# Kernel tuning notes

Measured on AMD Instinct MI355X. Metric: run time of the kernel, lower is better.

Reference implementation:

```python
import jax, jax.numpy as jnp
import numpy as np

N, D, H = 8192, 256, 128
KEEP_RATIO = 0.5
TEMP = 1.0
COS_EPS = 1e-4  # torch CosineSimilarity eps
NEG = -9e15


def setup_inputs() -> dict:
    key = jax.random.key(0)
    k1, k2, k3, k4 = jax.random.split(key, 4)
    features = jax.random.normal(k1, (N, D), dtype=jnp.float32)
    adj = jax.random.randint(k2, (N, N), 0, 2, dtype=jnp.int32)
    # module init: Linear weights ~ N(0, 0.001)
    Wq = jax.random.normal(k3, (H, D), dtype=jnp.float32) * 0.001
    Wk = jax.random.normal(k4, (H, D), dtype=jnp.float32) * 0.001
    return {"features": features, "adj": adj, "Wq": Wq, "Wk": Wk}


def _cos_normalize(x):
    # torch cosine: x / max(||x||, eps)
    n = jnp.linalg.norm(x, axis=-1, keepdims=True)
    return x / jnp.maximum(n, COS_EPS)


def reference(features, adj, Wq, Wk):
    # projections [N, H]
    Qn = _cos_normalize(features @ Wq.T)
    Kn = _cos_normalize(features @ Wk.T)
    # raw_att[i, j] = cos(Wq f_j, Wk f_i)  -> [N, N]
    raw_att = Kn @ Qn.T
    att = jnp.where(adj > 0, raw_att, NEG) * TEMP
    att = jax.nn.softmax(att, axis=1)
    prop_fea = att @ features  # [N, D]
    # nodes with no neighbors keep their own features
    adj_mask = (jnp.sum(adj, axis=1) > 0).astype(features.dtype)[:, None]
    prop_fea = adj_mask * prop_fea + (1.0 - adj_mask) * features
    # gate=None branch: fixed keep_ratio mixing
    return (1.0 - KEEP_RATIO) * prop_fea + KEEP_RATIO * features
```

## Files before the change

kernel.cpp:

```cpp
#include <hip/hip_runtime.h>
#include <stdint.h>
#include <stddef.h>

#define NN 8192
#define DD 256
#define HH 128

typedef short bf16x8 __attribute__((ext_vector_type(8)));
typedef float f32x4  __attribute__((ext_vector_type(4)));
typedef int   i32x4  __attribute__((ext_vector_type(4)));

static __device__ __forceinline__ short f2bf(float x){
  unsigned u = __float_as_uint(x);
  u = (u + 0x7FFFu + ((u >> 16) & 1u)) >> 16;
  return (short)(unsigned short)u;
}

static __device__ __forceinline__ bf16x8 cvt8(const float* p){
  f32x4 a = *(const f32x4*)p;
  f32x4 b = *(const f32x4*)(p + 4);
  bf16x8 o;
  o[0]=f2bf(a[0]); o[1]=f2bf(a[1]); o[2]=f2bf(a[2]); o[3]=f2bf(a[3]);
  o[4]=f2bf(b[0]); o[5]=f2bf(b[1]); o[6]=f2bf(b[2]); o[7]=f2bf(b[3]);
  return o;
}

static __device__ __forceinline__ bf16x8 ld16(const void* p){
  i32x4 v = *(const i32x4*)p;
  return __builtin_bit_cast(bf16x8, v);
}

__global__ __launch_bounds__(256) void k_transpose(const float* __restrict__ f,
                                                   unsigned short* __restrict__ ft){
  __shared__ unsigned short tile[64][65];
  int t  = threadIdx.x;
  int i0 = blockIdx.x * 64, d0 = blockIdx.y * 64;
  int r0 = t >> 6, c = t & 63;
  for (int it = 0; it < 16; ++it){
    int r = r0 + it * 4;
    tile[c][r] = (unsigned short)f2bf(f[(size_t)(i0 + r) * DD + d0 + c]);
  }
  __syncthreads();
  for (int it = 0; it < 16; ++it){
    int rr = r0 + it * 4;
    ft[(size_t)(d0 + rr) * NN + i0 + c] = tile[rr][c];
  }
}

__global__ __launch_bounds__(256) void k_proj(const float* __restrict__ f,
                                              const float* __restrict__ Wq,
                                              const float* __restrict__ Wk,
                                              unsigned short* __restrict__ Qn,
                                              unsigned short* __restrict__ Kn){
  int t = threadIdx.x, wave = t >> 6, l = t & 63;
  int i0 = blockIdx.x * 64 + wave * 16;
  int lr = l & 15, lk = l >> 4;
  bf16x8 ka[8];
  for (int ks = 0; ks < 8; ++ks)
    ka[ks] = cvt8(f + (size_t)(i0 + lr) * DD + ks * 32 + lk * 8);
  for (int pj = 0; pj < 2; ++pj){
    const float* W = pj ? Wk : Wq;
    unsigned short* out = pj ? Kn : Qn;
    f32x4 acc[8];
    for (int n = 0; n < 8; ++n) acc[n] = (f32x4){0.f,0.f,0.f,0.f};
    for (int ks = 0; ks < 8; ++ks)
      for (int n = 0; n < 8; ++n){
        bf16x8 bb = cvt8(W + (size_t)(n * 16 + lr) * DD + ks * 32 + lk * 8);
        acc[n] = __builtin_amdgcn_mfma_f32_16x16x32_bf16(ka[ks], bb, acc[n], 0, 0, 0);
      }
    for (int r = 0; r < 4; ++r){
      float n2 = 0.f;
      for (int n = 0; n < 8; ++n){ float v = acc[n][r]; n2 += v * v; }
      n2 += __shfl_xor(n2, 1); n2 += __shfl_xor(n2, 2);
      n2 += __shfl_xor(n2, 4); n2 += __shfl_xor(n2, 8);
      float s = 1.f / fmaxf(sqrtf(n2), 1e-4f);
      int row = i0 + lk * 4 + r;
      for (int n = 0; n < 8; ++n)
        out[(size_t)row * HH + n * 16 + lr] = (unsigned short)f2bf(acc[n][r] * s);
    }
  }
}

__global__ __launch_bounds__(256, 2) void k_attn(const int* __restrict__ adj,
      const unsigned short* __restrict__ Qn, const unsigned short* __restrict__ Kn,
      const unsigned short* __restrict__ ft,
      float* __restrict__ num_p, float* __restrict__ den_p){
  __shared__ __align__(16) char smem[57344];
  char* qn_s = smem;
  char* ft_s = smem + 16384;
  char* w_s  = smem + 49152;
  int t = threadIdx.x, wave = t >> 6, l = t & 63;
  int ib = blockIdx.x >> 2, js = blockIdx.x & 3;
  int i0 = ib * 64;
  int jbase = js * 2048;
  int lr = l & 15, lk = l >> 4;
  int swz = (l & 7) << 4;
  bf16x8 ka[4];
  {
    const unsigned short* kp = Kn + (size_t)(i0 + wave * 16 + lr) * HH;
    for (int ks = 0; ks < 4; ++ks) ka[ks] = ld16(kp + ks * 32 + lk * 8);
  }
  f32x4 pv[2][8];
  for (int a = 0; a < 2; ++a) for (int b = 0; b < 8; ++b) pv[a][b] = (f32x4){0.f,0.f,0.f,0.f};
  float dacc[4] = {0.f, 0.f, 0.f, 0.f};
  int rgp = wave & 1, dh = wave >> 1;
  int qrow = t >> 4, qc = t & 15;
  int frow = t >> 3, fc = t & 7;

  for (int step = 0; step < 32; ++step){
    int j0 = jbase + step * 64;
    __syncthreads();
    for (int it = 0; it < 4; ++it){
      int r = qrow + it * 16;
      i32x4 v = *(const i32x4*)(Qn + (size_t)(j0 + r) * HH + qc * 8);
      *(i32x4*)(qn_s + r * 256 + ((qc * 16) ^ ((r & 7) << 4))) = v;
    }
    for (int it = 0; it < 8; ++it){
      int d2 = frow + it * 32;
      i32x4 v = *(const i32x4*)(ft + (size_t)d2 * NN + j0 + fc * 8);
      *(i32x4*)(ft_s + d2 * 128 + ((fc * 16) ^ ((d2 & 7) << 4))) = v;
    }
    int adjv[4][4];
    for (int r = 0; r < 4; ++r){
      const int* ap = adj + (size_t)(i0 + wave * 16 + lk * 4 + r) * NN + j0 + lr;
      for (int cg = 0; cg < 4; ++cg)
        adjv[cg][r] = __builtin_nontemporal_load(ap + cg * 16);
    }
    __syncthreads();
    f32x4 sa[4];
    for (int cg = 0; cg < 4; ++cg) sa[cg] = (f32x4){0.f,0.f,0.f,0.f};
    for (int ks = 0; ks < 4; ++ks){
      int kb = (ks * 64 + lk * 16) ^ swz;
      for (int cg = 0; cg < 4; ++cg){
        bf16x8 bq = ld16(qn_s + (cg * 16 + lr) * 256 + kb);
        sa[cg] = __builtin_amdgcn_mfma_f32_16x16x32_bf16(ka[ks], bq, sa[cg], 0, 0, 0);
      }
    }
    for (int cg = 0; cg < 4; ++cg)
      for (int r = 0; r < 4; ++r){
        float w = adjv[cg][r] > 0 ? __expf(sa[cg][r]) : 0.f;
        dacc[r] += w;
        int row = wave * 16 + lk * 4 + r;
        *(unsigned short*)(w_s + row * 128 + ((cg * 32 + lr * 2) ^ ((row & 7) << 4)))
            = (unsigned short)f2bf(w);
      }
    __syncthreads();
    for (int ks = 0; ks < 2; ++ks){
      int kb = (ks * 64 + lk * 16) ^ swz;
      bf16x8 a0 = ld16(w_s + (rgp * 32 + lr) * 128 + kb);
      bf16x8 a1 = ld16(w_s + (rgp * 32 + 16 + lr) * 128 + kb);
      for (int dn = 0; dn < 8; ++dn){
        int dl = dh * 128 + dn * 16 + lr;
        bf16x8 bv = ld16(ft_s + dl * 128 + kb);
        pv[0][dn] = __builtin_amdgcn_mfma_f32_16x16x32_bf16(a0, bv, pv[0][dn], 0, 0, 0);
        pv[1][dn] = __builtin_amdgcn_mfma_f32_16x16x32_bf16(a1, bv, pv[1][dn], 0, 0, 0);
      }
    }
  }
  for (int r = 0; r < 4; ++r){
    float v = dacc[r];
    v += __shfl_xor(v, 1); v += __shfl_xor(v, 2);
    v += __shfl_xor(v, 4); v += __shfl_xor(v, 8);
    if (lr == 0) den_p[(size_t)js * NN + i0 + wave * 16 + lk * 4 + r] = v;
  }
  float* np = num_p + (size_t)js * NN * DD;
  for (int rgi = 0; rgi < 2; ++rgi)
    for (int dn = 0; dn < 8; ++dn)
      for (int r = 0; r < 4; ++r){
        int row = i0 + rgp * 32 + rgi * 16 + lk * 4 + r;
        int col = dh * 128 + dn * 16 + lr;
        np[(size_t)row * DD + col] = pv[rgi][dn][r];
      }
}

__global__ __launch_bounds__(256) void k_final(const float* __restrict__ num_p,
                                               const float* __restrict__ den_p,
                                               const float* __restrict__ f,
                                               float* __restrict__ out){
  int gid = blockIdx.x * 256 + threadIdx.x;
  int i = gid >> 6;
  f32x4 nv = (f32x4){0.f,0.f,0.f,0.f};
  float dv = 0.f;
  for (int s = 0; s < 4; ++s){
    nv += *(const f32x4*)(num_p + (size_t)s * NN * DD + (size_t)gid * 4);
    dv += den_p[(size_t)s * NN + i];
  }
  f32x4 fv = *(const f32x4*)(f + (size_t)gid * 4);
  f32x4 o;
  if (dv > 0.f){
    float inv = 0.5f / dv;
    o = nv * inv + fv * 0.5f;
  } else {
    o = fv;
  }
  *(f32x4*)(out + (size_t)gid * 4) = o;
}

extern "C" void kernel_launch(void* const* d_in, const int* in_sizes, int n_in,
                              void* d_out, int out_size, void* d_ws, size_t ws_size,
                              hipStream_t stream){
  (void)in_sizes; (void)n_in; (void)out_size;
  const float* feat = (const float*)d_in[0];
  const int*   adj  = (const int*)d_in[1];
  const float* Wq   = (const float*)d_in[2];
  const float* Wk   = (const float*)d_in[3];
  float* out = (float*)d_out;
  char* ws = (char*)d_ws;
  unsigned short* Qn = (unsigned short*)(ws);
  unsigned short* Kn = (unsigned short*)(ws + (2u << 20));
  unsigned short* ft = (unsigned short*)(ws + (4u << 20));
  float* num_p = (float*)(ws + (8u << 20));
  float* den_p = (float*)(ws + (40u << 20));
  if (ws_size < (40u << 20) + (4u * NN * 4u)) return;

  k_transpose<<<dim3(128, 4), 256, 0, stream>>>(feat, ft);
  k_proj<<<128, 256, 0, stream>>>(feat, Wq, Wk, Qn, Kn);
  k_attn<<<512, 256, 0, stream>>>(adj, Qn, Kn, ft, num_p, den_p);
  k_final<<<2048, 256, 0, stream>>>(num_p, den_p, feat, out);
}
```

Baseline: 233.0 us.

## Pre-fragment Q and features for direct MFMA loads and double-buffer adj

Qn and the transposed features are written in MFMA-fragment order so the attention kernel loads its operands straight from global memory into registers, dropping the per-step LDS staging of Q and features. The kernel switches to 32x32x16 MFMA tiles, keeps only the probability tile in shared memory, and prefetches the next step's adj values into a second register buffer. The denominator partials are split per j-group, so eight slices are written instead of four. The aim is to cut LDS traffic and barrier stalls and to hide adj load latency, at the cost of more registers and uncoalesced reads from global memory or L2.

```diff
diff --git a/kernel.cpp b/kernel.cpp
--- a/kernel.cpp
+++ b/kernel.cpp
@@ -6,16 +6,16 @@
 #define DD 256
 #define HH 128
 
-typedef short bf16x8 __attribute__((ext_vector_type(8)));
-typedef float f32x4  __attribute__((ext_vector_type(4)));
-typedef int   i32x4  __attribute__((ext_vector_type(4)));
+typedef short bf16x8  __attribute__((ext_vector_type(8)));
+typedef float f32x4   __attribute__((ext_vector_type(4)));
+typedef float f32x16  __attribute__((ext_vector_type(16)));
+typedef int   i32x4   __attribute__((ext_vector_type(4)));
 
 static __device__ __forceinline__ short f2bf(float x){
   unsigned u = __float_as_uint(x);
   u = (u + 0x7FFFu + ((u >> 16) & 1u)) >> 16;
   return (short)(unsigned short)u;
 }
-
 static __device__ __forceinline__ bf16x8 cvt8(const float* p){
   f32x4 a = *(const f32x4*)p;
   f32x4 b = *(const f32x4*)(p + 4);
@@ -24,153 +24,169 @@
   o[4]=f2bf(b[0]); o[5]=f2bf(b[1]); o[6]=f2bf(b[2]); o[7]=f2bf(b[3]);
   return o;
 }
-
 static __device__ __forceinline__ bf16x8 ld16(const void* p){
   i32x4 v = *(const i32x4*)p;
   return __builtin_bit_cast(bf16x8, v);
 }
 
-__global__ __launch_bounds__(256) void k_transpose(const float* __restrict__ f,
-                                                   unsigned short* __restrict__ ft){
-  __shared__ unsigned short tile[64][65];
-  int t  = threadIdx.x;
-  int i0 = blockIdx.x * 64, d0 = blockIdx.y * 64;
-  int r0 = t >> 6, c = t & 63;
-  for (int it = 0; it < 16; ++it){
-    int r = r0 + it * 4;
-    tile[c][r] = (unsigned short)f2bf(f[(size_t)(i0 + r) * DD + d0 + c]);
-  }
-  __syncthreads();
-  for (int it = 0; it < 16; ++it){
-    int rr = r0 + it * 4;
-    ft[(size_t)(d0 + rr) * NN + i0 + c] = tile[rr][c];
-  }
+__global__ __launch_bounds__(256) void k_ftfrag(const float* __restrict__ f,
+                                                unsigned short* __restrict__ ftf){
+  int t = threadIdx.x;
+  int fr = blockIdx.x * 4 + (t >> 6);
+  int l  = t & 63;
+  int jt = fr >> 3, dt = fr & 7;
+  int j = jt * 16 + (l >> 5) * 8, d = dt * 32 + (l & 31);
+  bf16x8 o;
+  #pragma unroll
+  for (int e = 0; e < 8; ++e) o[e] = f2bf(f[(size_t)(j + e) * DD + d]);
+  *(bf16x8*)(ftf + (size_t)fr * 512 + l * 8) = o;
 }
 
 __global__ __launch_bounds__(256) void k_proj(const float* __restrict__ f,
                                               const float* __restrict__ Wq,
                                               const float* __restrict__ Wk,
-                                              unsigned short* __restrict__ Qn,
+                                              unsigned short* __restrict__ Qnf,
                                               unsigned short* __restrict__ Kn){
   int t = threadIdx.x, wave = t >> 6, l = t & 63;
   int i0 = blockIdx.x * 64 + wave * 16;
   int lr = l & 15, lk = l >> 4;
   bf16x8 ka[8];
+  #pragma unroll
   for (int ks = 0; ks < 8; ++ks)
     ka[ks] = cvt8(f + (size_t)(i0 + lr) * DD + ks * 32 + lk * 8);
   for (int pj = 0; pj < 2; ++pj){
     const float* W = pj ? Wk : Wq;
-    unsigned short* out = pj ? Kn : Qn;
     f32x4 acc[8];
+    #pragma unroll
     for (int n = 0; n < 8; ++n) acc[n] = (f32x4){0.f,0.f,0.f,0.f};
     for (int ks = 0; ks < 8; ++ks)
+      #pragma unroll
       for (int n = 0; n < 8; ++n){
         bf16x8 bb = cvt8(W + (size_t)(n * 16 + lr) * DD + ks * 32 + lk * 8);
         acc[n] = __builtin_amdgcn_mfma_f32_16x16x32_bf16(ka[ks], bb, acc[n], 0, 0, 0);
       }
+    #pragma unroll
     for (int r = 0; r < 4; ++r){
       float n2 = 0.f;
+      #pragma unroll
       for (int n = 0; n < 8; ++n){ float v = acc[n][r]; n2 += v * v; }
       n2 += __shfl_xor(n2, 1); n2 += __shfl_xor(n2, 2);
       n2 += __shfl_xor(n2, 4); n2 += __shfl_xor(n2, 8);
       float s = 1.f / fmaxf(sqrtf(n2), 1e-4f);
       int row = i0 + lk * 4 + r;
-      for (int n = 0; n < 8; ++n)
-        out[(size_t)row * HH + n * 16 + lr] = (unsigned short)f2bf(acc[n][r] * s);
+      #pragma unroll
+      for (int n = 0; n < 8; ++n){
+        short v = f2bf(acc[n][r] * s);
+        if (pj){
+          Kn[(size_t)row * HH + n * 16 + lr] = (unsigned short)v;
+        } else {
+          size_t off = ((size_t)(row >> 5) * 8 + n) * 512
+                     + ((row & 31) + 32 * (lr >> 3)) * 8 + (lr & 7);
+          Qnf[off] = (unsigned short)v;
+        }
+      }
     }
   }
 }
 
-__global__ __launch_bounds__(256, 2) void k_attn(const int* __restrict__ adj,
-      const unsigned short* __restrict__ Qn, const unsigned short* __restrict__ Kn,
-      const unsigned short* __restrict__ ft,
+#define STEP(CUR, NXT, SS) {                                                      \
+  const int j0 = jbase + (SS) * 64;                                               \
+  const int jn = ((SS) < 31) ? j0 + 64 : j0;                                      \
+  _Pragma("unroll")                                                               \
+  for (int r = 0; r < 16; ++r)                                                    \
+    NXT[r] = __builtin_nontemporal_load(                                          \
+        adj + (size_t)(iA + (r & 3) + 8 * (r >> 2)) * NN + jn + jg * 32 + lc);    \
+  f32x16 st;                                                                      \
+  _Pragma("unroll") for (int e = 0; e < 16; ++e) st[e] = 0.f;                     \
+  { const unsigned short* qb = Qnf + ((size_t)((j0 + jg * 32) >> 5) * 8) * 512 + (size_t)l * 8; \
+    _Pragma("unroll")                                                             \
+    for (int hs = 0; hs < 8; ++hs)                                                \
+      st = __builtin_amdgcn_mfma_f32_32x32x16_bf16(kb[hs], ld16(qb + hs * 512), st, 0, 0, 0); } \
+  bf16x8 bv[8];                                                                   \
+  { const unsigned short* fb = ftf + ((size_t)(j0 >> 4) * 8 + wq * 2) * 512 + (size_t)l * 8; \
+    _Pragma("unroll")                                                             \
+    for (int ks = 0; ks < 4; ++ks){                                               \
+      bv[ks * 2]     = ld16(fb + ks * 4096);                                      \
+      bv[ks * 2 + 1] = ld16(fb + ks * 4096 + 512); } }                            \
+  _Pragma("unroll")                                                               \
+  for (int r = 0; r < 16; ++r){                                                   \
+    float wv = (CUR[r] > 0) ? __expf(st[r]) : 0.f;          \
+    dacc[r] += wv;                                                                \
+    int row = ig * 32 + (r & 3) + 8 * (r >> 2) + 4 * h;                           \
+    int byo = row * 128 + (((jg * 32 + lc) * 2) ^ ((row & 7) << 4));              \
+    *(unsigned short*)(p_lds + byo) = (unsigned short)f2bf(wv);                   \
+  }                                                                               \
+  __syncthreads();                                                                \
+  _Pragma("unroll")                                                               \
+  for (int ks = 0; ks < 4; ++ks){                                                 \
+    int ko = (ks * 32 + h * 16) ^ ((lc & 7) << 4);                                \
+    bf16x8 pa0 = ld16(p_lds + lc * 128 + ko);                                     \
+    bf16x8 pa1 = ld16(p_lds + (32 + lc) * 128 + ko);                              \
+    pv00 = __builtin_amdgcn_mfma_f32_32x32x16_bf16(pa0, bv[ks*2],   pv00, 0,0,0); \
+    pv01 = __builtin_amdgcn_mfma_f32_32x32x16_bf16(pa0, bv[ks*2+1], pv01, 0,0,0); \
+    pv10 = __builtin_amdgcn_mfma_f32_32x32x16_bf16(pa1, bv[ks*2],   pv10, 0,0,0); \
+    pv11 = __builtin_amdgcn_mfma_f32_32x32x16_bf16(pa1, bv[ks*2+1], pv11, 0,0,0); \
+  }                                                                               \
+  __syncthreads();                                                                \
+}
+
+__global__ __launch_bounds__(256, 2) void k_attn(
+      const int* __restrict__ adj,
+      const unsigned short* __restrict__ Qnf, const unsigned short* __restrict__ Kn,
+      const unsigned short* __restrict__ ftf,
       float* __restrict__ num_p, float* __restrict__ den_p){
-  __shared__ __align__(16) char smem[57344];
-  char* qn_s = smem;
-  char* ft_s = smem + 16384;
-  char* w_s  = smem + 49152;
+  __shared__ __attribute__((aligned(16))) char p_lds[8192];
   int t = threadIdx.x, wave = t >> 6, l = t & 63;
+  int lc = l & 31, h = l >> 5;
+  int ig = wave >> 1, jg = wave & 1, wq = wave;
   int ib = blockIdx.x >> 2, js = blockIdx.x & 3;
   int i0 = ib * 64;
   int jbase = js * 2048;
-  int lr = l & 15, lk = l >> 4;
-  int swz = (l & 7) << 4;
-  bf16x8 ka[4];
-  {
-    const unsigned short* kp = Kn + (size_t)(i0 + wave * 16 + lr) * HH;
-    for (int ks = 0; ks < 4; ++ks) ka[ks] = ld16(kp + ks * 32 + lk * 8);
-  }
-  f32x4 pv[2][8];
-  for (int a = 0; a < 2; ++a) for (int b = 0; b < 8; ++b) pv[a][b] = (f32x4){0.f,0.f,0.f,0.f};
-  float dacc[4] = {0.f, 0.f, 0.f, 0.f};
-  int rgp = wave & 1, dh = wave >> 1;
-  int qrow = t >> 4, qc = t & 15;
-  int frow = t >> 3, fc = t & 7;
-
-  for (int step = 0; step < 32; ++step){
-    int j0 = jbase + step * 64;
-    __syncthreads();
-    for (int it = 0; it < 4; ++it){
-      int r = qrow + it * 16;
-      i32x4 v = *(const i32x4*)(Qn + (size_t)(j0 + r) * HH + qc * 8);
-      *(i32x4*)(qn_s + r * 256 + ((qc * 16) ^ ((r & 7) << 4))) = v;
+  int iA = i0 + ig * 32 + 4 * h;
+
+  bf16x8 kb[8];
+  { const unsigned short* kp = Kn + (size_t)(i0 + ig * 32 + lc) * HH + h * 8;
+    #pragma unroll
+    for (int hs = 0; hs < 8; ++hs) kb[hs] = ld16(kp + hs * 16); }
+
+  f32x16 pv00, pv01, pv10, pv11;
+  #pragma unroll
+  for (int e = 0; e < 16; ++e){ pv00[e]=0.f; pv01[e]=0.f; pv10[e]=0.f; pv11[e]=0.f; }
+  float dacc[16];
+  #pragma unroll
+  for (int r = 0; r < 16; ++r) dacc[r] = 0.f;
+
+  int adjA[16], adjB[16];
+  #pragma unroll
+  for (int r = 0; r < 16; ++r)
+    adjA[r] = __builtin_nontemporal_load(
+        adj + (size_t)(iA + (r & 3) + 8 * (r >> 2)) * NN + jbase + jg * 32 + lc);
+
+  for (int sp = 0; sp < 16; ++sp){
+    STEP(adjA, adjB, 2 * sp)
+    STEP(adjB, adjA, 2 * sp + 1)
+  }
+
+  #pragma unroll
+  for (int r = 0; r < 16; ++r){
+    float v = dacc[r];
+    v += __shfl_xor(v, 1); v += __shfl_xor(v, 2); v += __shfl_xor(v, 4);
+    v += __shfl_xor(v, 8); v += __shfl_xor(v, 16);
+    if (lc == 0){
+      int i = i0 + ig * 32 + (r & 3) + 8 * (r >> 2) + 4 * h;
+      den_p[(size_t)(js * 2 + jg) * NN + i] = v;
     }
-    for (int it = 0; it < 8; ++it){
-      int d2 = frow + it * 32;
-      i32x4 v = *(const i32x4*)(ft + (size_t)d2 * NN + j0 + fc * 8);
-      *(i32x4*)(ft_s + d2 * 128 + ((fc * 16) ^ ((d2 & 7) << 4))) = v;
-    }
-    int adjv[4][4];
-    for (int r = 0; r < 4; ++r){
-      const int* ap = adj + (size_t)(i0 + wave * 16 + lk * 4 + r) * NN + j0 + lr;
-      for (int cg = 0; cg < 4; ++cg)
-        adjv[cg][r] = __builtin_nontemporal_load(ap + cg * 16);
-    }
-    __syncthreads();
-    f32x4 sa[4];
-    for (int cg = 0; cg < 4; ++cg) sa[cg] = (f32x4){0.f,0.f,0.f,0.f};
-    for (int ks = 0; ks < 4; ++ks){
-      int kb = (ks * 64 + lk * 16) ^ swz;
-      for (int cg = 0; cg < 4; ++cg){
-        bf16x8 bq = ld16(qn_s + (cg * 16 + lr) * 256 + kb);
-        sa[cg] = __builtin_amdgcn_mfma_f32_16x16x32_bf16(ka[ks], bq, sa[cg], 0, 0, 0);
-      }
-    }
-    for (int cg = 0; cg < 4; ++cg)
-      for (int r = 0; r < 4; ++r){
-        float w = adjv[cg][r] > 0 ? __expf(sa[cg][r]) : 0.f;
-        dacc[r] += w;
-        int row = wave * 16 + lk * 4 + r;
-        *(unsigned short*)(w_s + row * 128 + ((cg * 32 + lr * 2) ^ ((row & 7) << 4)))
-            = (unsigned short)f2bf(w);
-      }
-    __syncthreads();
-    for (int ks = 0; ks < 2; ++ks){
-      int kb = (ks * 64 + lk * 16) ^ swz;
-      bf16x8 a0 = ld16(w_s + (rgp * 32 + lr) * 128 + kb);
-      bf16x8 a1 = ld16(w_s + (rgp * 32 + 16 + lr) * 128 + kb);
-      for (int dn = 0; dn < 8; ++dn){
-        int dl = dh * 128 + dn * 16 + lr;
-        bf16x8 bv = ld16(ft_s + dl * 128 + kb);
-        pv[0][dn] = __builtin_amdgcn_mfma_f32_16x16x32_bf16(a0, bv, pv[0][dn], 0, 0, 0);
-        pv[1][dn] = __builtin_amdgcn_mfma_f32_16x16x32_bf16(a1, bv, pv[1][dn], 0, 0, 0);
-      }
-    }
-  }
-  for (int r = 0; r < 4; ++r){
-    float v = dacc[r];
-    v += __shfl_xor(v, 1); v += __shfl_xor(v, 2);
-    v += __shfl_xor(v, 4); v += __shfl_xor(v, 8);
-    if (lr == 0) den_p[(size_t)js * NN + i0 + wave * 16 + lk * 4 + r] = v;
   }
   float* np = num_p + (size_t)js * NN * DD;
-  for (int rgi = 0; rgi < 2; ++rgi)
-    for (int dn = 0; dn < 8; ++dn)
-      for (int r = 0; r < 4; ++r){
-        int row = i0 + rgp * 32 + rgi * 16 + lk * 4 + r;
-        int col = dh * 128 + dn * 16 + lr;
-        np[(size_t)row * DD + col] = pv[rgi][dn][r];
-      }
+  #pragma unroll
+  for (int r = 0; r < 16; ++r){
+    int i = i0 + (r & 3) + 8 * (r >> 2) + 4 * h;
+    int d = wq * 64 + lc;
+    np[(size_t)i * DD + d]             = pv00[r];
+    np[(size_t)i * DD + d + 32]        = pv01[r];
+    np[(size_t)(i + 32) * DD + d]      = pv10[r];
+    np[(size_t)(i + 32) * DD + d + 32] = pv11[r];
+  }
 }
 
 __global__ __launch_bounds__(256) void k_final(const float* __restrict__ num_p,
@@ -181,10 +197,12 @@
   int i = gid >> 6;
   f32x4 nv = (f32x4){0.f,0.f,0.f,0.f};
   float dv = 0.f;
-  for (int s = 0; s < 4; ++s){
+  #pragma unroll
+  for (int s = 0; s < 4; ++s)
     nv += *(const f32x4*)(num_p + (size_t)s * NN * DD + (size_t)gid * 4);
+  #pragma unroll
+  for (int s = 0; s < 8; ++s)
     dv += den_p[(size_t)s * NN + i];
-  }
   f32x4 fv = *(const f32x4*)(f + (size_t)gid * 4);
   f32x4 o;
   if (dv > 0.f){
@@ -206,15 +224,15 @@
   const float* Wk   = (const float*)d_in[3];
   float* out = (float*)d_out;
   char* ws = (char*)d_ws;
-  unsigned short* Qn = (unsigned short*)(ws);
-  unsigned short* Kn = (unsigned short*)(ws + (2u << 20));
-  unsigned short* ft = (unsigned short*)(ws + (4u << 20));
-  float* num_p = (float*)(ws + (8u << 20));
-  float* den_p = (float*)(ws + (40u << 20));
-  if (ws_size < (40u << 20) + (4u * NN * 4u)) return;
-
-  k_transpose<<<dim3(128, 4), 256, 0, stream>>>(feat, ft);
-  k_proj<<<128, 256, 0, stream>>>(feat, Wq, Wk, Qn, Kn);
-  k_attn<<<512, 256, 0, stream>>>(adj, Qn, Kn, ft, num_p, den_p);
+  unsigned short* Qnf  = (unsigned short*)(ws);
+  unsigned short* Kn   = (unsigned short*)(ws + (2u << 20));
+  unsigned short* ftf  = (unsigned short*)(ws + (4u << 20));
+  float*          num_p = (float*)(ws + (8u << 20));
+  float*          den_p = (float*)(ws + (40u << 20));
+  if (ws_size < (40u << 20) + 262144u) return;
+
+  k_ftfrag<<<1024, 256, 0, stream>>>(feat, ftf);
+  k_proj<<<128, 256, 0, stream>>>(feat, Wq, Wk, Qnf, Kn);
+  k_attn<<<512, 256, 0, stream>>>(adj, Qnf, Kn, ftf, num_p, den_p);
   k_final<<<2048, 256, 0, stream>>>(num_p, den_p, feat, out);
 }
```

New measurement: 235.6 us. About the same (+1.1%).
